# Kernel tuning notes

Hardware: AMD Instinct MI355X
Metric: run time of the kernel (lower is better)

The kernel has to match this reference:

```python
import jax, jax.numpy as jnp
import numpy as np

GRID_SIZE = 5
SPLINE_ORDER = 3
B, D, O = 16384, 512, 512


def _make_grid():
    h = 2.0 / GRID_SIZE
    # matches torch.arange(-k, grid_size + k + 1) * h - 2.0  -> 12 knots
    return jnp.arange(-SPLINE_ORDER, GRID_SIZE + SPLINE_ORDER + 1, dtype=jnp.float32) * h - 2.0


def _bspline_basis(x, grid):
    # x: [B, D]; grid: [G] with G = grid_size + 2*order + 1 = 12
    G = grid.shape[0]
    xe = x[..., None]                      # [B, D, 1]
    g = grid.reshape(1, 1, G)              # [1, 1, G]
    # degree-0: indicator of knot interval  -> [B, D, G-1]
    bases = ((xe >= g[:, :, :-1]) & (xe < g[:, :, 1:])).astype(x.dtype)
    eps = 1e-9
    for k in range(1, SPLINE_ORDER + 1):   # Cox-de Boor recursion, width shrinks by 1 each step
        left = (xe - g[:, :, :-k - 1]) / (g[:, :, k:-1] - g[:, :, :-k - 1] + eps)
        right = (g[:, :, k + 1:] - xe) / (g[:, :, k + 1:] - g[:, :, 1:-k] + eps)
        bases = left * bases[..., :-1] + right * bases[..., 1:]
    return bases                           # [B, D, grid_size + order] = [B, D, 8]


def setup_inputs() -> dict:
    key = jax.random.key(0)
    k1, k2, k3 = jax.random.split(key, 3)
    x = jax.random.normal(k1, (B, D), dtype=jnp.float32)
    # kaiming_uniform_(a=sqrt(5)*0.1): bound = sqrt(6 / ((1 + a^2) * fan_in))
    a = np.sqrt(5.0) * 0.1
    bound = float(np.sqrt(6.0 / ((1.0 + a * a) * D)))
    base_weight = jax.random.uniform(k2, (O, D), dtype=jnp.float32, minval=-bound, maxval=bound)
    spline_weight = jax.random.normal(k3, (O, D, GRID_SIZE + SPLINE_ORDER), dtype=jnp.float32) * 0.01
    return {"x": x, "base_weight": base_weight, "spline_weight": spline_weight}


def reference(x, base_weight, spline_weight):
    grid = _make_grid()
    base_output = jnp.matmul(jax.nn.silu(x), base_weight.T)      # [B, O]
    x_norm = jnp.clip(x, -2.0, 2.0)
    basis = _bspline_basis(x_norm, grid)                          # [B, D, 8]
    spline_output = jnp.einsum('bic,oic->bo', basis, spline_weight)
    return base_output + spline_output
```

## Files before the change

### kernel.cpp

```cpp
#include <hip/hip_runtime.h>
#include <cstdint>
#include <cstddef>
#include <type_traits>

#define B_ROWS 16384
#define D_DIM  512
#define O_DIM  512
#define K_DIM  4608
#define BM 128
#define BN 256
#define BK 32

typedef __bf16 bf16;
typedef __attribute__((ext_vector_type(8))) bf16  bf16x8;
typedef __attribute__((ext_vector_type(4))) float f32x4;

__device__ __forceinline__ void async_load16(const void* g, void* l) {
    __builtin_amdgcn_global_load_lds(
        (const __attribute__((address_space(1))) void*)g,
        (__attribute__((address_space(3))) void*)l,
        16, 0, 0);
}

__device__ __forceinline__ uint32_t pk2(float a, float b) {
    uint16_t ua = __builtin_bit_cast(uint16_t, (__bf16)a);
    uint16_t ub = __builtin_bit_cast(uint16_t, (__bf16)b);
    return (uint32_t)ua | ((uint32_t)ub << 16);
}

__device__ __forceinline__ void spline_pairs(float xv, uint32_t out[4]) {
    float xn = fminf(fmaxf(xv, -2.0f), 2.0f);
    float t  = (xn + 3.2f) * 2.5f;
    int   j0 = (int)t;
    float u  = t - (float)j0;
    float u2 = u * u, u3 = u2 * u, omu = 1.0f - u;
    const float s6 = 1.0f / 6.0f;
    float w0 = omu * omu * omu * s6;
    float w1 = (3.0f * u3 - 6.0f * u2 + 4.0f) * s6;
    float w2 = (-3.0f * u3 + 3.0f * u2 + 3.0f * u + 1.0f) * s6;
    float w3 = u3 * s6;
    uint64_t W64 = ((uint64_t)pk2(w2, w3) << 32) | pk2(w0, w1);
    int sh = (j0 - 3) * 16;
    uint64_t lo = W64 << (sh & 63);
    uint64_t hi = W64 >> ((64 - sh) & 63);
    uint32_t lo_lo = (uint32_t)lo, lo_hi = (uint32_t)(lo >> 32);
    uint32_t hi_lo = (uint32_t)hi, hi_hi = (uint32_t)(hi >> 32);
    bool lt64 = sh < 64, eq0 = (sh == 0), lt128 = sh < 128;
    out[0] = lt64 ? lo_lo : 0u;
    out[1] = lt64 ? lo_hi : 0u;
    out[2] = lt64 ? (eq0 ? 0u : hi_lo) : (lt128 ? lo_lo : 0u);
    out[3] = lt64 ? (eq0 ? 0u : hi_hi) : (lt128 ? lo_hi : 0u);
}

__global__ void pack_w_kernel(const float* __restrict__ bw,
                              const float* __restrict__ sw,
                              bf16* __restrict__ W) {
    int idx = blockIdx.x * blockDim.x + threadIdx.x;
    if (idx >= O_DIM * 64) return;
    int o  = idx >> 6;
    int i0 = (idx & 63) * 8;

    bf16 ob[9][8];
    const float* bwp = bw + (size_t)o * D_DIM + i0;
#pragma unroll
    for (int e = 0; e < 8; e++) {
        ob[0][e] = (bf16)bwp[e];
        const float* sp = sw + ((size_t)o * D_DIM + i0 + e) * 8;
#pragma unroll
        for (int c = 0; c < 8; c++)
            ob[c + 1][e] = (bf16)sp[c];
    }
    bf16* row = W + (size_t)o * K_DIM + i0;
#pragma unroll
    for (int f = 0; f < 9; f++)
        *(bf16x8*)(row + (size_t)f * D_DIM) = *(const bf16x8*)ob[f];
}

#define BARW(n) asm volatile("s_waitcnt vmcnt(" #n ") lgkmcnt(0)\n\ts_barrier" ::: "memory")

__global__ __launch_bounds__(512, 2)
void gemm_fused_kernel(const float* __restrict__ x, const bf16* __restrict__ W,
                       float* __restrict__ C) {
    __shared__ __align__(16) bf16 As0[BM * BK], As1[BM * BK], As2[BM * BK], As3[BM * BK];
    __shared__ __align__(16) bf16 Bs0[BN * BK], Bs1[BN * BK], Bs2[BN * BK];
    __shared__ __align__(16) bf16 Bs3[BN * BK], Bs4[BN * BK], Bs5[BN * BK];

    const int tid  = threadIdx.x;
    const int bid  = blockIdx.x;
    const int n0   = (bid & 1) * BN;
    const int m0   = (bid >> 1) * BM;
    const int wave = tid >> 6;
    const int lane = tid & 63;
    const int wm   = (wave >> 2) * 64;
    const int wn   = (wave & 3) * 64;
    const int l15  = lane & 15;
    const int quad = lane >> 4;
    const int swz  = (l15 >> 1) & 3;
    const int aoff = l15 * BK + (quad ^ swz) * 8;
    const int boff = (wn + l15) * BK + (quad ^ swz) * 8;

    const int rA = tid >> 2;
    const int q8 = tid & 3;
    const float* xrow = x + (size_t)(m0 + rA) * D_DIM + q8 * 8;
    const int awo = rA * BK + ((q8 ^ ((rA >> 1) & 3)) * 8);

    const bf16* gB = W + (size_t)(n0 + (tid >> 2)) * K_DIM
                       + (((tid & 3) ^ ((tid >> 3) & 3)) * 8);

    bf16* const AsArr[4] = {As0, As1, As2, As3};
    bf16* const BsArr[6] = {Bs0, Bs1, Bs2, Bs3, Bs4, Bs5};

    f32x4 acc[4][4] = {};
    uint32_t vpk[2][4][8];
    float xe[8];

    auto write_pack = [&](bf16* slab, const uint32_t (&P)[4][8], int j) {
        const int pr = j >> 1;
        uint32_t o[4];
#pragma unroll
        for (int m = 0; m < 4; m++) {
            uint32_t lo = P[pr][2*m], hi = P[pr][2*m+1];
            o[m] = (j & 1) ? ((lo >> 16) | (hi & 0xFFFF0000u))
                           : ((lo & 0xFFFFu) | (hi << 16));
        }
        *(uint4*)(slab + awo) = *(const uint4*)o;
    };
    auto write_silu = [&](bf16* slab) {
        float sl[8];
#pragma unroll
        for (int e = 0; e < 8; e++)
            sl[e] = xe[e] * __builtin_amdgcn_rcpf(1.0f + __expf(-xe[e]));
        uint32_t o[4] = {pk2(sl[0],sl[1]), pk2(sl[2],sl[3]),
                         pk2(sl[4],sl[5]), pk2(sl[6],sl[7])};
        *(uint4*)(slab + awo) = *(const uint4*)o;
    };

    {
        float4 a = *(const float4*)xrow;
        float4 b = *(const float4*)(xrow + 4);
        xe[0]=a.x; xe[1]=a.y; xe[2]=a.z; xe[3]=a.w;
        xe[4]=b.x; xe[5]=b.y; xe[6]=b.z; xe[7]=b.w;
#pragma unroll
        for (int F = 0; F < 4; F++) {
            const bf16* src = gB + (size_t)(F * 512);
            async_load16(src,                       BsArr[F] + tid * 8);
            async_load16(src + (size_t)128 * K_DIM, BsArr[F] + tid * 8 + 4096);
        }
#pragma unroll
        for (int e = 0; e < 8; e++) {
            uint32_t o4[4];
            spline_pairs(xe[e], o4);
            vpk[0][0][e]=o4[0]; vpk[0][1][e]=o4[1];
            vpk[0][2][e]=o4[2]; vpk[0][3][e]=o4[3];
        }
        write_silu(As0);
        write_pack(As1, vpk[0], 0);
        BARW(4);
    }

    auto step_body = [&](auto c4v, auto fv, int c) {
        constexpr int C4 = decltype(c4v)::value;
        constexpr int F  = decltype(fv)::value;
        constexpr int PC = C4 & 1;
        constexpr int BR = (3 * PC + F) % 6;
        constexpr int BW = (3 * PC + F + 4) % 6;
        constexpr int AR = (C4 + F) & 3;
        constexpr int AW = (C4 + F + 2) & 3;

        if (F == 0 && c < 15) {
            float4 a = *(const float4*)(xrow + (c + 1) * 32);
            float4 b = *(const float4*)(xrow + (c + 1) * 32 + 4);
            xe[0]=a.x; xe[1]=a.y; xe[2]=a.z; xe[3]=a.w;
            xe[4]=b.x; xe[5]=b.y; xe[6]=b.z; xe[7]=b.w;
        }
        {
            constexpr int f2 = (F + 4 <= 8) ? (F + 4) : (F - 5);
            const int c2 = (F + 4 <= 8) ? c : (c + 1);
            if (c2 < 16) {
                const bf16* src = gB + (size_t)(f2 * 512 + c2 * 32);
                async_load16(src,                       BsArr[BW] + tid * 8);
                async_load16(src + (size_t)128 * K_DIM, BsArr[BW] + tid * 8 + 4096);
            }
        }
        bf16x8 af[4], bfr[4];
#pragma unroll
        for (int tt = 0; tt < 4; tt++)
            af[tt] = *(const bf16x8*)(AsArr[AR] + (wm + tt * 16) * BK + aoff);
#pragma unroll
        for (int tt = 0; tt < 4; tt++)
            bfr[tt] = *(const bf16x8*)(BsArr[BR] + boff + tt * 16 * BK);

        if (F >= 1 && c < 15) {
            uint32_t o4[4];
            spline_pairs(xe[F - 1], o4);
            vpk[PC ^ 1][0][F-1]=o4[0]; vpk[PC ^ 1][1][F-1]=o4[1];
            vpk[PC ^ 1][2][F-1]=o4[2]; vpk[PC ^ 1][3][F-1]=o4[3];
        }
        if constexpr (F <= 6) {
            write_pack(AsArr[AW], vpk[PC], F + 1);
        } else if constexpr (F == 7) {
            if (c < 15) write_silu(AsArr[AW]);
        } else {
            if (c < 15) write_pack(AsArr[AW], vpk[PC ^ 1], 0);
        }

        __builtin_amdgcn_s_setprio(1);
#pragma unroll
        for (int im = 0; im < 4; im++)
#pragma unroll
            for (int jn = 0; jn < 4; jn++)
                acc[im][jn] = __builtin_amdgcn_mfma_f32_16x16x32_bf16(
                    af[im], bfr[jn], acc[im][jn], 0, 0, 0);
        __builtin_amdgcn_s_setprio(0);

        if constexpr (((PC + F) & 1) == 1) {
            if constexpr (PC == 0 && F == 1) {
                BARW(6);
            } else if constexpr (PC == 1 && F == 0) {
                if (c < 15) { BARW(6); } else { BARW(4); }
            } else if constexpr (F == 8) {
                if (c != 15) BARW(4);
            } else if constexpr (F == 6) {
                if (c == 15) { BARW(0); } else { BARW(4); }
            } else {
                BARW(4);
            }
        }
    };

#define IC(n) std::integral_constant<int,(n)>{}
    auto chunk_body = [&](auto c4v, int c) {
        step_body(c4v, IC(0), c); step_body(c4v, IC(1), c); step_body(c4v, IC(2), c);
        step_body(c4v, IC(3), c); step_body(c4v, IC(4), c); step_body(c4v, IC(5), c);
        step_body(c4v, IC(6), c); step_body(c4v, IC(7), c); step_body(c4v, IC(8), c);
    };

    for (int cc = 0; cc < 16; cc += 4) {
        chunk_body(IC(0), cc);
        chunk_body(IC(1), cc + 1);
        chunk_body(IC(2), cc + 2);
        chunk_body(IC(3), cc + 3);
    }
#undef IC

#pragma unroll
    for (int im = 0; im < 4; im++) {
        const int rbase = m0 + wm + im * 16 + quad * 4;
#pragma unroll
        for (int jn = 0; jn < 4; jn++) {
            const int col = n0 + wn + jn * 16 + l15;
#pragma unroll
            for (int rr = 0; rr < 4; rr++)
                C[(size_t)(rbase + rr) * O_DIM + col] = acc[im][jn][rr];
        }
    }
}

extern "C" void kernel_launch(void* const* d_in, const int* in_sizes, int n_in,
                              void* d_out, int out_size, void* d_ws, size_t ws_size,
                              hipStream_t stream) {
    const float* x  = (const float*)d_in[0];
    const float* bw = (const float*)d_in[1];
    const float* sw = (const float*)d_in[2];
    float* out = (float*)d_out;

    const size_t Wbytes = (size_t)O_DIM * K_DIM * sizeof(bf16);
    if (ws_size < Wbytes) return;
    bf16* W = (bf16*)d_ws;

    pack_w_kernel<<<(O_DIM * 64 + 255) / 256, 256, 0, stream>>>(bw, sw, W);
    gemm_fused_kernel<<<dim3(B_ROWS / BM * (O_DIM / BN)), dim3(512), 0, stream>>>(x, W, out);
}
```

Before: 170.1 us.

## Pre-swizzle weights into MFMA fragment layout and load B directly into registers

The weight packer now writes W in a fragment-major layout, so each lane's MFMA B operand is one contiguous 16-byte global load. The GEMM drops the six LDS B buffers and async global-to-LDS copies, and instead double-buffers B fragments in registers (brA/brB), prefetched one step ahead. Barriers now wait only on LDS counters since B no longer goes through shared memory. This removes LDS traffic and footprint for B, but each wave reads B straight from global/L2 with no sharing across waves, and there is more register pressure and exposed global latency.

Measured after the change: 167.9 us. Within noise of the previous version (-1.3%).

```diff
diff --git a/kernel.cpp b/kernel.cpp
--- a/kernel.cpp
+++ b/kernel.cpp
@@ -6,7 +6,6 @@
 #define B_ROWS 16384
 #define D_DIM  512
 #define O_DIM  512
-#define K_DIM  4608
 #define BM 128
 #define BN 256
 #define BK 32
@@ -14,13 +13,6 @@
 typedef __bf16 bf16;
 typedef __attribute__((ext_vector_type(8))) bf16  bf16x8;
 typedef __attribute__((ext_vector_type(4))) float f32x4;
-
-__device__ __forceinline__ void async_load16(const void* g, void* l) {
-    __builtin_amdgcn_global_load_lds(
-        (const __attribute__((address_space(1))) void*)g,
-        (__attribute__((address_space(3))) void*)l,
-        16, 0, 0);
-}
 
 __device__ __forceinline__ uint32_t pk2(float a, float b) {
     uint16_t ua = __builtin_bit_cast(uint16_t, (__bf16)a);
@@ -70,20 +62,23 @@
         for (int c = 0; c < 8; c++)
             ob[c + 1][e] = (bf16)sp[c];
     }
-    bf16* row = W + (size_t)o * K_DIM + i0;
-#pragma unroll
-    for (int f = 0; f < 9; f++)
-        *(bf16x8*)(row + (size_t)f * D_DIM) = *(const bf16x8*)ob[f];
-}
-
-#define BARW(n) asm volatile("s_waitcnt vmcnt(" #n ") lgkmcnt(0)\n\ts_barrier" ::: "memory")
+    const int c   = i0 >> 5;
+    const int sub = (i0 & 31) >> 3;
+    const int cb  = o >> 4;
+    const int ln  = (o & 15) + sub * 16;
+#pragma unroll
+    for (int f = 0; f < 9; f++) {
+        size_t off = ((size_t)((f * 16 + c) * 32 + cb) * 64 + ln) * 8;
+        *(bf16x8*)(W + off) = *(const bf16x8*)ob[f];
+    }
+}
+
+#define BARA asm volatile("s_waitcnt lgkmcnt(0)\n\ts_barrier" ::: "memory")
 
 __global__ __launch_bounds__(512, 2)
-void gemm_fused_kernel(const float* __restrict__ x, const bf16* __restrict__ W,
+void gemm_fused_kernel(const float* __restrict__ x, const bf16* __restrict__ Wf,
                        float* __restrict__ C) {
     __shared__ __align__(16) bf16 As0[BM * BK], As1[BM * BK], As2[BM * BK], As3[BM * BK];
-    __shared__ __align__(16) bf16 Bs0[BN * BK], Bs1[BN * BK], Bs2[BN * BK];
-    __shared__ __align__(16) bf16 Bs3[BN * BK], Bs4[BN * BK], Bs5[BN * BK];
 
     const int tid  = threadIdx.x;
     const int bid  = blockIdx.x;
@@ -97,20 +92,18 @@
     const int quad = lane >> 4;
     const int swz  = (l15 >> 1) & 3;
     const int aoff = l15 * BK + (quad ^ swz) * 8;
-    const int boff = (wn + l15) * BK + (quad ^ swz) * 8;
 
     const int rA = tid >> 2;
     const int q8 = tid & 3;
     const float* xrow = x + (size_t)(m0 + rA) * D_DIM + q8 * 8;
     const int awo = rA * BK + ((q8 ^ ((rA >> 1) & 3)) * 8);
 
-    const bf16* gB = W + (size_t)(n0 + (tid >> 2)) * K_DIM
-                       + (((tid & 3) ^ ((tid >> 3) & 3)) * 8);
+    const bf16* gBf = Wf + ((size_t)(((n0 + wn) >> 4) * 64 + lane)) * 8;
 
     bf16* const AsArr[4] = {As0, As1, As2, As3};
-    bf16* const BsArr[6] = {Bs0, Bs1, Bs2, Bs3, Bs4, Bs5};
 
     f32x4 acc[4][4] = {};
+    bf16x8 brA[4], brB[4];
     uint32_t vpk[2][4][8];
     float xe[8];
 
@@ -136,16 +129,13 @@
     };
 
     {
+#pragma unroll
+        for (int jn = 0; jn < 4; jn++)
+            brA[jn] = *(const bf16x8*)(gBf + jn * 512);
         float4 a = *(const float4*)xrow;
         float4 b = *(const float4*)(xrow + 4);
         xe[0]=a.x; xe[1]=a.y; xe[2]=a.z; xe[3]=a.w;
         xe[4]=b.x; xe[5]=b.y; xe[6]=b.z; xe[7]=b.w;
-#pragma unroll
-        for (int F = 0; F < 4; F++) {
-            const bf16* src = gB + (size_t)(F * 512);
-            async_load16(src,                       BsArr[F] + tid * 8);
-            async_load16(src + (size_t)128 * K_DIM, BsArr[F] + tid * 8 + 4096);
-        }
 #pragma unroll
         for (int e = 0; e < 8; e++) {
             uint32_t o4[4];
@@ -155,15 +145,14 @@
         }
         write_silu(As0);
         write_pack(As1, vpk[0], 0);
-        BARW(4);
+        BARA;
     }
 
     auto step_body = [&](auto c4v, auto fv, int c) {
         constexpr int C4 = decltype(c4v)::value;
         constexpr int F  = decltype(fv)::value;
         constexpr int PC = C4 & 1;
-        constexpr int BR = (3 * PC + F) % 6;
-        constexpr int BW = (3 * PC + F + 4) % 6;
+        constexpr int TP = (C4 + F) & 1;
         constexpr int AR = (C4 + F) & 3;
         constexpr int AW = (C4 + F + 2) & 3;
 
@@ -173,22 +162,23 @@
             xe[0]=a.x; xe[1]=a.y; xe[2]=a.z; xe[3]=a.w;
             xe[4]=b.x; xe[5]=b.y; xe[6]=b.z; xe[7]=b.w;
         }
-        {
-            constexpr int f2 = (F + 4 <= 8) ? (F + 4) : (F - 5);
-            const int c2 = (F + 4 <= 8) ? c : (c + 1);
-            if (c2 < 16) {
-                const bf16* src = gB + (size_t)(f2 * 512 + c2 * 32);
-                async_load16(src,                       BsArr[BW] + tid * 8);
-                async_load16(src + (size_t)128 * K_DIM, BsArr[BW] + tid * 8 + 4096);
+        if (!(c == 15 && F == 8)) {
+            const int tN = (F < 8) ? ((F + 1) * 16 + c) : (c + 1);
+            const bf16* src = gBf + (size_t)tN * 16384;
+            if constexpr (TP == 0) {
+#pragma unroll
+                for (int jn = 0; jn < 4; jn++)
+                    brB[jn] = *(const bf16x8*)(src + jn * 512);
+            } else {
+#pragma unroll
+                for (int jn = 0; jn < 4; jn++)
+                    brA[jn] = *(const bf16x8*)(src + jn * 512);
             }
         }
-        bf16x8 af[4], bfr[4];
+        bf16x8 af[4];
 #pragma unroll
         for (int tt = 0; tt < 4; tt++)
             af[tt] = *(const bf16x8*)(AsArr[AR] + (wm + tt * 16) * BK + aoff);
-#pragma unroll
-        for (int tt = 0; tt < 4; tt++)
-            bfr[tt] = *(const bf16x8*)(BsArr[BR] + boff + tt * 16 * BK);
 
         if (F >= 1 && c < 15) {
             uint32_t o4[4];
@@ -210,21 +200,11 @@
 #pragma unroll
             for (int jn = 0; jn < 4; jn++)
                 acc[im][jn] = __builtin_amdgcn_mfma_f32_16x16x32_bf16(
-                    af[im], bfr[jn], acc[im][jn], 0, 0, 0);
+                    af[im], (TP == 0) ? brA[jn] : brB[jn], acc[im][jn], 0, 0, 0);
         __builtin_amdgcn_s_setprio(0);
 
-        if constexpr (((PC + F) & 1) == 1) {
-            if constexpr (PC == 0 && F == 1) {
-                BARW(6);
-            } else if constexpr (PC == 1 && F == 0) {
-                if (c < 15) { BARW(6); } else { BARW(4); }
-            } else if constexpr (F == 8) {
-                if (c != 15) BARW(4);
-            } else if constexpr (F == 6) {
-                if (c == 15) { BARW(0); } else { BARW(4); }
-            } else {
-                BARW(4);
-            }
+        if constexpr (TP == 1) {
+            if (!(c == 15 && F == 8)) BARA;
         }
     };
 
@@ -264,7 +244,7 @@
     const float* sw = (const float*)d_in[2];
     float* out = (float*)d_out;
 
-    const size_t Wbytes = (size_t)O_DIM * K_DIM * sizeof(bf16);
+    const size_t Wbytes = (size_t)144 * 32 * 64 * 8 * sizeof(bf16);
     if (ws_size < Wbytes) return;
     bf16* W = (bf16*)d_ws;
 
```
